# Kernel tuning notes

Measured on AMD Instinct MI355X. Metric: run time of the kernel, lower is better.

Reference implementation:

```python
import jax, jax.numpy as jnp
import numpy as np

B, S, D, H, DH = 4, 2048, 512, 8, 64

def setup_inputs() -> dict:
    key = jax.random.key(0)
    k1, k2, k3, k4 = jax.random.split(key, 4)
    sc = 1.0 / np.sqrt(D)
    return {
        "x": jax.random.normal(k1, (B, S, D), dtype=jnp.float32),
        "Wq": jax.random.normal(k2, (H, D, DH), dtype=jnp.float32) * sc,
        "Wk": jax.random.normal(k3, (H, D, DH), dtype=jnp.float32) * sc,
        "Wv": jax.random.normal(k4, (H, D, DH), dtype=jnp.float32) * sc,
    }

def reference(x, Wq, Wk, Wv):
    # x: [B,S,D]; Wq/Wk/Wv: [H,D,DH] (stacked per-head bias-free Linear weights)
    q = jnp.einsum('bsd,hdk->bhsk', x, Wq)
    k = jnp.einsum('bsd,hdk->bhsk', x, Wk)
    v = jnp.einsum('bsd,hdk->bhsk', x, Wv)
    scale = DH ** -0.5
    scores = jax.nn.softmax(jnp.einsum('bhqk,bhsk->bhqs', q, k) * scale, axis=-1)
    out = jnp.einsum('bhqs,bhsk->bhqk', scores, v)  # [B,H,S,DH]
    # concat heads along last dim (head order matches ModuleList order)
    return out.transpose(0, 2, 1, 3).reshape(B, S, H * DH)
```

## Files before the change

kernel.cpp:

```cpp
#include <hip/hip_runtime.h>

typedef _Float16 half8  __attribute__((ext_vector_type(8)));
typedef _Float16 half4v __attribute__((ext_vector_type(4)));
typedef _Float16 half2v __attribute__((ext_vector_type(2)));
typedef __fp16   fp16x2 __attribute__((ext_vector_type(2)));
typedef float    float4v __attribute__((ext_vector_type(4)));

#define CSC 0.18033688f

__device__ __forceinline__ void async16(const _Float16* g, void* l) {
    __builtin_amdgcn_global_load_lds((const __attribute__((address_space(1))) void*)g,
                                     (__attribute__((address_space(3))) void*)l, 16, 0, 0);
}

__device__ __forceinline__ half2v pk2(float a, float b) {
    return __builtin_bit_cast(half2v, __builtin_amdgcn_cvt_pkrtz(a, b));
}

__global__ __launch_bounds__(256) void mha_prep(const float* __restrict__ x,
    const float* __restrict__ wq, const float* __restrict__ wk, const float* __restrict__ wv,
    _Float16* __restrict__ xh, _Float16* __restrict__ wt) {
    __shared__ __align__(16) _Float16 T[64][72];
    const int tid = threadIdx.x;
    if (blockIdx.x < 4096) {
        int t = blockIdx.x * 256 + tid;
        float4v v = ((const float4v*)x)[t];
        half4v o;
        #pragma unroll
        for (int i = 0; i < 4; ++i) o[i] = (_Float16)v[i];
        ((half4v*)xh)[t] = o;
        return;
    }
    const int blk = blockIdx.x - 4096;
    const int dt = blk & 7, h = (blk >> 3) & 7, mat = blk >> 6;
    const float* w = ((mat == 0) ? wq : (mat == 1) ? wk : wv) + h * 32768 + dt * 64 * 64;
    #pragma unroll
    for (int i = 0; i < 4; ++i) {
        int s = tid + i * 256;
        int dl = s >> 4, c4 = s & 15;
        float4v v = ((const float4v*)(w + (size_t)dl * 64))[c4];
        #pragma unroll
        for (int e = 0; e < 4; ++e) T[c4 * 4 + e][dl] = (_Float16)v[e];
    }
    __syncthreads();
    #pragma unroll
    for (int i = 0; i < 2; ++i) {
        int s = tid + i * 256;
        int dh = s >> 3, c8 = s & 7;
        half8 o;
        #pragma unroll
        for (int e = 0; e < 8; ++e) o[e] = T[dh][c8 * 8 + e];
        *(half8*)(wt + (size_t)((mat * 8 + h) * 64 + dh) * 512 + dt * 64 + c8 * 8) = o;
    }
}

__global__ __launch_bounds__(256, 3) void mha_qkv(const _Float16* __restrict__ xh,
    const _Float16* __restrict__ wt, _Float16* __restrict__ Qm, _Float16* __restrict__ Km,
    _Float16* __restrict__ Vt) {
    __shared__ __align__(16) char smem[34816];
    _Float16* Ash[2] = { (_Float16*)smem,           (_Float16*)(smem + 8192)  };
    _Float16* Bsh[2] = { (_Float16*)(smem + 16384), (_Float16*)(smem + 24576) };
    const int tid = threadIdx.x;
    const int lane = tid & 63, wave = tid >> 6;
    const int quad = lane >> 4, li = lane & 15;
    const int m0 = blockIdx.x * 128, n0 = blockIdx.y * 128;
    float4v acc[4][4] = {};
    const int r0 = tid >> 2, c0 = (tid & 3) ^ ((r0 >> 1) & 3);
    const int s1 = 256 + tid, r1 = s1 >> 2, c1 = (s1 & 3) ^ ((r1 >> 1) & 3);
    const _Float16* gA0 = xh + (size_t)(m0 + r0) * 512 + c0 * 8;
    const _Float16* gA1 = xh + (size_t)(m0 + r1) * 512 + c1 * 8;
    const _Float16* gB0 = wt + (size_t)(n0 + r0) * 512 + c0 * 8;
    const _Float16* gB1 = wt + (size_t)(n0 + r1) * 512 + c1 * 8;
    const int wr = (wave >> 1) * 64, wc = (wave & 1) * 64;
    const char* aB[2]; const char* bB[2];
    #pragma unroll
    for (int bb = 0; bb < 2; ++bb) {
        aB[bb] = (const char*)Ash[bb] + (wr + li) * 64 + ((quad ^ ((li >> 1) & 3)) << 4);
        bB[bb] = (const char*)Bsh[bb] + (wc + li) * 64 + ((quad ^ ((li >> 1) & 3)) << 4);
    }
    auto stage = [&](int bb, int kk) {
        async16(gA0 + kk, (char*)Ash[bb] + wave * 1024);
        async16(gA1 + kk, (char*)Ash[bb] + 4096 + wave * 1024);
        async16(gB0 + kk, (char*)Bsh[bb] + wave * 1024);
        async16(gB1 + kk, (char*)Bsh[bb] + 4096 + wave * 1024);
    };
    auto compute = [&](int bb) {
        half8 af[4], bf[4];
        #pragma unroll
        for (int mt = 0; mt < 4; ++mt) af[mt] = *(const half8*)(aB[bb] + mt * 1024);
        #pragma unroll
        for (int nt = 0; nt < 4; ++nt) bf[nt] = *(const half8*)(bB[bb] + nt * 1024);
        #pragma unroll
        for (int mt = 0; mt < 4; ++mt)
            #pragma unroll
            for (int nt = 0; nt < 4; ++nt)
                acc[mt][nt] = __builtin_amdgcn_mfma_f32_16x16x32_f16(af[mt], bf[nt], acc[mt][nt], 0, 0, 0);
    };
    stage(0, 0);
    for (int kk = 0; kk < 512; kk += 64) {
        __syncthreads();
        stage(1, kk + 32);
        compute(0);
        __syncthreads();
        if (kk + 64 < 512) stage(0, kk + 64);
        compute(1);
    }
    const int mat = n0 >> 9;
    if (mat == 2) {
        #pragma unroll
        for (int mt = 0; mt < 4; ++mt) {
            int m = m0 + wr + mt * 16 + quad * 4;
            int b = m >> 11, s = m & 2047;
            #pragma unroll
            for (int nt = 0; nt < 4; ++nt) {
                int n = n0 + wc + nt * 16 + li;
                int h = (n >> 6) & 7, dh = n & 63;
                int bh = b * 8 + h;
                half4v pkv;
                #pragma unroll
                for (int r = 0; r < 4; ++r) pkv[r] = (_Float16)acc[mt][nt][r];
                *(half4v*)(Vt + ((size_t)bh * 64 + dh) * 2048 + s) = pkv;
            }
        }
    } else {
        _Float16* dst = (mat == 0) ? Qm : Km;
        const float osc = (mat == 0) ? CSC : 1.0f;
        __syncthreads();
        char* Tb = smem;
        #pragma unroll
        for (int mt = 0; mt < 4; ++mt) {
            int rbase = wr + mt * 16 + quad * 4;
            #pragma unroll
            for (int nt = 0; nt < 4; ++nt) {
                int col = wc + nt * 16 + li;
                #pragma unroll
                for (int r = 0; r < 4; ++r)
                    *(_Float16*)(Tb + (rbase + r) * 272 + col * 2) = (_Float16)(acc[mt][nt][r] * osc);
            }
        }
        __syncthreads();
        const int h0 = (n0 >> 6) & 7;
        #pragma unroll
        for (int i = 0; i < 8; ++i) {
            int c = i * 256 + tid;
            int row = c >> 4, j8 = c & 15;
            half8 v = *(const half8*)(Tb + row * 272 + j8 * 16);
            int m = m0 + row;
            int b = m >> 11, s = m & 2047;
            int bh = b * 8 + h0 + (j8 >> 3);
            *(half8*)(dst + ((size_t)bh * 2048 + s) * 64 + (j8 & 7) * 8) = v;
        }
    }
}

__global__ __launch_bounds__(256, 2) void mha_attn(const _Float16* __restrict__ Qm,
    const _Float16* __restrict__ Km, const _Float16* __restrict__ Vt, float* __restrict__ out) {
    __shared__ __align__(16) char mrg[40960];
    const int tid = threadIdx.x, lane = tid & 63, wave = tid >> 6;
    const int quad = lane >> 4, li = lane & 15;
    const int strm = wave & 1, hh = wave >> 1;
    const int flat = blockIdx.x;
    const int xcd = flat & 7, n = flat >> 3;
    const int bh = xcd * 4 + (n & 3);
    const int qb = n >> 2;
    const int b = bh >> 3, h = bh & 7;
    const _Float16* Qg = Qm + (size_t)bh * 2048 * 64;
    const _Float16* Kg = Km + (size_t)bh * 2048 * 64 + (size_t)strm * 1024 * 64;
    const _Float16* Vg = Vt + (size_t)bh * 64 * 2048 + (size_t)strm * 1024;
    const int q0 = qb * 128 + hh * 64;
    half8 qf[4][2];
    #pragma unroll
    for (int qt = 0; qt < 4; ++qt)
        #pragma unroll
        for (int ds = 0; ds < 2; ++ds)
            qf[qt][ds] = *(const half8*)(Qg + (size_t)(q0 + qt * 16 + li) * 64 + ds * 32 + quad * 8);
    half8 vone;
    #pragma unroll
    for (int e = 0; e < 8; ++e) vone[e] = (_Float16)1.0f;
    float4v O[4][4] = {};
    float4v O4[4] = {};
    const int rE = ((li >> 2) << 3) | (li & 3);
    const _Float16* kRow = Kg + (size_t)rE * 64 + quad * 8;
    const _Float16* vRow = Vg + (size_t)li * 2048 + quad * 8;
    #pragma unroll 2
    for (int t = 0; t < 16; ++t) {
        const int kb = t * 64;
        #pragma unroll
        for (int c = 0; c < 2; ++c) {
            const _Float16* kc = kRow + (size_t)(kb + c * 32) * 64;
            half8 f0e = *(const half8*)(kc);
            half8 f1e = *(const half8*)(kc + 32);
            half8 f0o = *(const half8*)(kc + 256);
            half8 f1o = *(const half8*)(kc + 288);
            half8 pf[4];
            #pragma unroll
            for (int qt = 0; qt < 4; ++qt) {
                float4v se = {}, so = {};
                __builtin_amdgcn_s_setprio(1);
                se = __builtin_amdgcn_mfma_f32_16x16x32_f16(f0e, qf[qt][0], se, 0, 0, 0);
                se = __builtin_amdgcn_mfma_f32_16x16x32_f16(f1e, qf[qt][1], se, 0, 0, 0);
                so = __builtin_amdgcn_mfma_f32_16x16x32_f16(f0o, qf[qt][0], so, 0, 0, 0);
                so = __builtin_amdgcn_mfma_f32_16x16x32_f16(f1o, qf[qt][1], so, 0, 0, 0);
                __builtin_amdgcn_s_setprio(0);
                float pe[4], po[4];
                #pragma unroll
                for (int r = 0; r < 4; ++r) {
                    pe[r] = __builtin_amdgcn_exp2f(se[r]);
                    po[r] = __builtin_amdgcn_exp2f(so[r]);
                }
                half4v a = __builtin_shufflevector(pk2(pe[0], pe[1]), pk2(pe[2], pe[3]), 0, 1, 2, 3);
                half4v o = __builtin_shufflevector(pk2(po[0], po[1]), pk2(po[2], po[3]), 0, 1, 2, 3);
                pf[qt] = __builtin_shufflevector(a, o, 0, 1, 2, 3, 4, 5, 6, 7);
            }
            __builtin_amdgcn_s_setprio(1);
            #pragma unroll
            for (int qt = 0; qt < 4; ++qt)
                O4[qt] = __builtin_amdgcn_mfma_f32_16x16x32_f16(pf[qt], vone, O4[qt], 0, 0, 0);
            #pragma unroll
            for (int dt = 0; dt < 4; ++dt) {
                half8 vf = *(const half8*)(vRow + (size_t)dt * 32768 + kb + c * 32);
                #pragma unroll
                for (int qt = 0; qt < 4; ++qt)
                    O[qt][dt] = __builtin_amdgcn_mfma_f32_16x16x32_f16(pf[qt], vf, O[qt][dt], 0, 0, 0);
            }
            __builtin_amdgcn_s_setprio(0);
        }
    }
    __syncthreads();
    float* Obuf = (float*)mrg;
    float* Lbuf = (float*)(mrg + 32768);
    if (strm == 1) {
        #pragma unroll
        for (int qt = 0; qt < 4; ++qt) {
            #pragma unroll
            for (int dt = 0; dt < 4; ++dt)
                ((float4v*)(Obuf + hh * 4096))[(qt * 4 + dt) * 64 + lane] = O[qt][dt];
            ((float4v*)(Lbuf + hh * 1024))[qt * 64 + lane] = O4[qt];
        }
    }
    __syncthreads();
    if (strm == 1) return;
    #pragma unroll
    for (int qt = 0; qt < 4; ++qt) {
        #pragma unroll
        for (int dt = 0; dt < 4; ++dt) {
            float4v o2 = ((float4v*)(Obuf + hh * 4096))[(qt * 4 + dt) * 64 + lane];
            O[qt][dt] += o2;
        }
        float4v l2 = ((float4v*)(Lbuf + hh * 1024))[qt * 64 + lane];
        O4[qt] += l2;
    }
    #pragma unroll
    for (int qt = 0; qt < 4; ++qt) {
        #pragma unroll
        for (int r = 0; r < 4; ++r) {
            float inv = 1.0f / O4[qt][r];
            int q = q0 + qt * 16 + quad * 4 + r;
            float* orow = out + ((size_t)(b * 2048 + q)) * 512 + h * 64;
            #pragma unroll
            for (int dt = 0; dt < 4; ++dt) orow[dt * 16 + li] = O[qt][dt][r] * inv;
        }
    }
}

extern "C" void kernel_launch(void* const* d_in, const int* in_sizes, int n_in,
                              void* d_out, int out_size, void* d_ws, size_t ws_size,
                              hipStream_t stream) {
    const float* x  = (const float*)d_in[0];
    const float* wq = (const float*)d_in[1];
    const float* wk = (const float*)d_in[2];
    const float* wv = (const float*)d_in[3];
    float* out = (float*)d_out;
    char* ws = (char*)d_ws;
    _Float16* xh = (_Float16*)(ws);
    _Float16* wt = (_Float16*)(ws + 8388608);
    _Float16* Qm = (_Float16*)(ws + 9961472);
    _Float16* Km = (_Float16*)(ws + 18350080);
    _Float16* Vt = (_Float16*)(ws + 26738688);
    if (ws_size < 35127296u) return;
    mha_prep<<<4288, 256, 0, stream>>>(x, wq, wk, wv, xh, wt);
    mha_qkv<<<dim3(64, 12), 256, 0, stream>>>(xh, wt, Qm, Km, Vt);
    mha_attn<<<512, 256, 0, stream>>>(Qm, Km, Vt, out);
}
```

Baseline: 156.9 us.

## Stage K/V tiles through swizzled LDS with async double-buffered loads

```diff
diff --git a/kernel.cpp b/kernel.cpp
--- a/kernel.cpp
+++ b/kernel.cpp
@@ -3,10 +3,13 @@
 typedef _Float16 half8  __attribute__((ext_vector_type(8)));
 typedef _Float16 half4v __attribute__((ext_vector_type(4)));
 typedef _Float16 half2v __attribute__((ext_vector_type(2)));
-typedef __fp16   fp16x2 __attribute__((ext_vector_type(2)));
 typedef float    float4v __attribute__((ext_vector_type(4)));
 
 #define CSC 0.18033688f
+
+#define WAITV8 asm volatile("s_waitcnt vmcnt(8)" ::: "memory")
+#define WAITV0 asm volatile("s_waitcnt vmcnt(0)" ::: "memory")
+#define WAITL0 asm volatile("s_waitcnt lgkmcnt(0)" ::: "memory")
 
 __device__ __forceinline__ void async16(const _Float16* g, void* l) {
     __builtin_amdgcn_global_load_lds((const __attribute__((address_space(1))) void*)g,
@@ -155,14 +158,13 @@
 
 __global__ __launch_bounds__(256, 2) void mha_attn(const _Float16* __restrict__ Qm,
     const _Float16* __restrict__ Km, const _Float16* __restrict__ Vt, float* __restrict__ out) {
-    __shared__ __align__(16) char mrg[40960];
+    __shared__ __align__(16) char smem[65536];
     const int tid = threadIdx.x, lane = tid & 63, wave = tid >> 6;
     const int quad = lane >> 4, li = lane & 15;
     const int strm = wave & 1, hh = wave >> 1;
     const int flat = blockIdx.x;
-    const int xcd = flat & 7, n = flat >> 3;
-    const int bh = xcd * 4 + (n & 3);
-    const int qb = n >> 2;
+    const int qb = (flat >> 3) & 15;
+    const int bh = ((flat >> 7) << 3) | (flat & 7);
     const int b = bh >> 3, h = bh & 7;
     const _Float16* Qg = Qm + (size_t)bh * 2048 * 64;
     const _Float16* Kg = Km + (size_t)bh * 2048 * 64 + (size_t)strm * 1024 * 64;
@@ -174,61 +176,100 @@
         #pragma unroll
         for (int ds = 0; ds < 2; ++ds)
             qf[qt][ds] = *(const half8*)(Qg + (size_t)(q0 + qt * 16 + li) * 64 + ds * 32 + quad * 8);
+    WAITV0;
     half8 vone;
     #pragma unroll
     for (int e = 0; e < 8; ++e) vone[e] = (_Float16)1.0f;
     float4v O[4][4] = {};
     float4v O4[4] = {};
-    const int rE = ((li >> 2) << 3) | (li & 3);
-    const _Float16* kRow = Kg + (size_t)rE * 64 + quad * 8;
-    const _Float16* vRow = Vg + (size_t)li * 2048 + quad * 8;
-    #pragma unroll 2
-    for (int t = 0; t < 16; ++t) {
-        const int kb = t * 64;
-        #pragma unroll
-        for (int c = 0; c < 2; ++c) {
-            const _Float16* kc = kRow + (size_t)(kb + c * 32) * 64;
-            half8 f0e = *(const half8*)(kc);
-            half8 f1e = *(const half8*)(kc + 32);
-            half8 f0o = *(const half8*)(kc + 256);
-            half8 f1o = *(const half8*)(kc + 288);
-            half8 pf[4];
-            #pragma unroll
-            for (int qt = 0; qt < 4; ++qt) {
-                float4v se = {}, so = {};
-                __builtin_amdgcn_s_setprio(1);
-                se = __builtin_amdgcn_mfma_f32_16x16x32_f16(f0e, qf[qt][0], se, 0, 0, 0);
-                se = __builtin_amdgcn_mfma_f32_16x16x32_f16(f1e, qf[qt][1], se, 0, 0, 0);
-                so = __builtin_amdgcn_mfma_f32_16x16x32_f16(f0o, qf[qt][0], so, 0, 0, 0);
-                so = __builtin_amdgcn_mfma_f32_16x16x32_f16(f1o, qf[qt][1], so, 0, 0, 0);
-                __builtin_amdgcn_s_setprio(0);
-                float pe[4], po[4];
-                #pragma unroll
-                for (int r = 0; r < 4; ++r) {
-                    pe[r] = __builtin_amdgcn_exp2f(se[r]);
-                    po[r] = __builtin_amdgcn_exp2f(so[r]);
-                }
-                half4v a = __builtin_shufflevector(pk2(pe[0], pe[1]), pk2(pe[2], pe[3]), 0, 1, 2, 3);
-                half4v o = __builtin_shufflevector(pk2(po[0], po[1]), pk2(po[2], po[3]), 0, 1, 2, 3);
-                pf[qt] = __builtin_shufflevector(a, o, 0, 1, 2, 3, 4, 5, 6, 7);
+    const int ls = lane >> 3, l7 = lane & 7;
+    const _Float16* pKe[2]; const _Float16* pKo[2]; const _Float16* pV[2];
+    pKe[0] = Kg + ls * 64 + ((l7 ^ (ls & 3)) << 3);
+    pKo[0] = Kg + (ls + 8) * 64 + (((l7 ^ (ls & 3)) ^ 4) << 3);
+    const int gsl = l7 ^ ls;
+    pV[0] = Vg + (size_t)(ls + ((gsl >> 2) << 5)) * 2048 + ((gsl & 3) << 3);
+    pKe[1] = pKe[0] + 2048;  pKo[1] = pKo[0] + 2048;  pV[1] = pV[0] + 32;
+    char* const base = smem + wave * 16384;
+    char* const dstK[2] = { base,        base + 8192  };
+    char* const dstV[2] = { base + 4096, base + 12288 };
+    const int rowE = ((li >> 2) << 3) | (li & 3);
+    const int swzE = (li & 3) | (((li >> 2) & 1) << 2);
+    const char *k0e[2], *k1e[2], *vB[2];
+    #pragma unroll
+    for (int bb = 0; bb < 2; ++bb) {
+        k0e[bb] = dstK[bb] + rowE * 128 + ((quad ^ swzE) << 4);
+        k1e[bb] = dstK[bb] + rowE * 128 + (((quad + 4) ^ swzE) << 4);
+        vB[bb]  = dstV[bb] + li * 128;
+    }
+    const int cV0 = (quad ^ (li & 7)) << 4;
+    const int cV1 = ((4 + quad) ^ (li & 7)) << 4;
+    auto stage = [&](int bb) {
+        async16(pKe[bb],         dstK[bb]);
+        async16(pKo[bb],         dstK[bb] + 1024);
+        async16(pKe[bb] + 1024,  dstK[bb] + 2048);
+        async16(pKo[bb] + 1024,  dstK[bb] + 3072);
+        async16(pV[bb],          dstV[bb]);
+        async16(pV[bb] + 16384,  dstV[bb] + 1024);
+        async16(pV[bb] + 32768,  dstV[bb] + 2048);
+        async16(pV[bb] + 49152,  dstV[bb] + 3072);
+        pKe[bb] += 4096; pKo[bb] += 4096; pV[bb] += 64;
+    };
+    auto tile = [&](int bb, bool doStage) {
+        half8 f0e = *(const half8*)(k0e[bb]);
+        half8 f1e = *(const half8*)(k1e[bb]);
+        half8 f0o = *(const half8*)(k0e[bb] + 512);
+        half8 f1o = *(const half8*)(k1e[bb] + 512);
+        half8 vf0 = *(const half8*)(vB[bb] + cV0);
+        half8 vf1 = *(const half8*)(vB[bb] + 2048 + cV0);
+        half8 vf2 = *(const half8*)(vB[bb] + cV1);
+        half8 vf3 = *(const half8*)(vB[bb] + 2048 + cV1);
+        WAITL0;
+        if (doStage) stage(bb);
+        half8 pf[4];
+        #pragma unroll
+        for (int qt = 0; qt < 4; ++qt) {
+            float4v se = {}, so = {};
+            __builtin_amdgcn_s_setprio(1);
+            se = __builtin_amdgcn_mfma_f32_16x16x32_f16(f0e, qf[qt][0], se, 0, 0, 0);
+            se = __builtin_amdgcn_mfma_f32_16x16x32_f16(f1e, qf[qt][1], se, 0, 0, 0);
+            so = __builtin_amdgcn_mfma_f32_16x16x32_f16(f0o, qf[qt][0], so, 0, 0, 0);
+            so = __builtin_amdgcn_mfma_f32_16x16x32_f16(f1o, qf[qt][1], so, 0, 0, 0);
+            __builtin_amdgcn_s_setprio(0);
+            float pe[4], po[4];
+            #pragma unroll
+            for (int r = 0; r < 4; ++r) {
+                pe[r] = __builtin_amdgcn_exp2f(se[r]);
+                po[r] = __builtin_amdgcn_exp2f(so[r]);
             }
-            __builtin_amdgcn_s_setprio(1);
-            #pragma unroll
-            for (int qt = 0; qt < 4; ++qt)
-                O4[qt] = __builtin_amdgcn_mfma_f32_16x16x32_f16(pf[qt], vone, O4[qt], 0, 0, 0);
-            #pragma unroll
-            for (int dt = 0; dt < 4; ++dt) {
-                half8 vf = *(const half8*)(vRow + (size_t)dt * 32768 + kb + c * 32);
-                #pragma unroll
-                for (int qt = 0; qt < 4; ++qt)
-                    O[qt][dt] = __builtin_amdgcn_mfma_f32_16x16x32_f16(pf[qt], vf, O[qt][dt], 0, 0, 0);
-            }
-            __builtin_amdgcn_s_setprio(0);
-        }
-    }
+            half4v a = __builtin_shufflevector(pk2(pe[0], pe[1]), pk2(pe[2], pe[3]), 0, 1, 2, 3);
+            half4v o = __builtin_shufflevector(pk2(po[0], po[1]), pk2(po[2], po[3]), 0, 1, 2, 3);
+            pf[qt] = __builtin_shufflevector(a, o, 0, 1, 2, 3, 4, 5, 6, 7);
+        }
+        __builtin_amdgcn_s_setprio(1);
+        #pragma unroll
+        for (int qt = 0; qt < 4; ++qt)
+            O4[qt] = __builtin_amdgcn_mfma_f32_16x16x32_f16(pf[qt], vone, O4[qt], 0, 0, 0);
+        #pragma unroll
+        for (int qt = 0; qt < 4; ++qt) {
+            O[qt][0] = __builtin_amdgcn_mfma_f32_16x16x32_f16(pf[qt], vf0, O[qt][0], 0, 0, 0);
+            O[qt][1] = __builtin_amdgcn_mfma_f32_16x16x32_f16(pf[qt], vf1, O[qt][1], 0, 0, 0);
+            O[qt][2] = __builtin_amdgcn_mfma_f32_16x16x32_f16(pf[qt], vf2, O[qt][2], 0, 0, 0);
+            O[qt][3] = __builtin_amdgcn_mfma_f32_16x16x32_f16(pf[qt], vf3, O[qt][3], 0, 0, 0);
+        }
+        __builtin_amdgcn_s_setprio(0);
+    };
+    stage(0);
+    stage(1);
+    #pragma unroll 1
+    for (int tp = 0; tp < 15; ++tp) {
+        WAITV8; tile(0, true);
+        WAITV8; tile(1, true);
+    }
+    WAITV8; tile(0, false);
+    WAITV0; tile(1, false);
     __syncthreads();
-    float* Obuf = (float*)mrg;
-    float* Lbuf = (float*)(mrg + 32768);
+    float* Obuf = (float*)smem;
+    float* Lbuf = (float*)(smem + 32768);
     if (strm == 1) {
         #pragma unroll
         for (int qt = 0; qt < 4; ++qt) {
```

After: 136.5 us. 1.15x faster.
